# Optimization experiments

Measured on AMD Instinct MI355X. Metric: run time of the kernel, lower is better.

The kernel has to match this reference:

```python
import jax, jax.numpy as jnp
import numpy as np

LAMBDA_ENTROPY = 0.1
LAMBDA_REPULSION = 0.5
LAMBDA_INTER = 0.3
TEMPERATURE = 1.0
EPS = 1e-8


def setup_inputs() -> dict:
    key = jax.random.key(0)
    k1, k2 = jax.random.split(key)
    membership = jax.random.uniform(k1, (16384, 64, 32), dtype=jnp.float32)   # (N,F,K) soft bin assignments
    teacher_preds = jax.random.uniform(k2, (16384, 128), dtype=jnp.float32)   # (N,C)
    return {"membership": membership, "teacher_preds": teacher_preds}


def reference(membership, teacher_preds):
    N, F, K = membership.shape
    # --- weighted centroids per (feature, bin) ---
    bin_mass = membership.sum(axis=0) + EPS                       # (F,K)
    sum_weighted_y = jnp.einsum('nfk,nc->fkc', membership, teacher_preds)  # avoids (N,F,K,C)
    centroids = sum_weighted_y / bin_mass[..., None]              # (F,K,C)
    # --- weighted intra-bin variance: ||y_n - c_fk||^2 expanded, no (N,F,K,C) tensor ---
    y_sq = jnp.sum(teacher_preds * teacher_preds, axis=-1)        # (N,)
    c_sq = jnp.sum(centroids * centroids, axis=-1)                # (F,K)
    cross = jnp.einsum('nc,fkc->nfk', teacher_preds, centroids)   # (N,F,K)
    dist_sq = y_sq[:, None, None] + c_sq[None, :, :] - 2.0 * cross
    weighted_variance = jnp.sum(membership * dist_sq, axis=0) / bin_mass  # (F,K)
    loss_dispersion = weighted_variance.sum()
    # --- bin-occupancy entropy ---
    p_bins = bin_mass / N                                         # (F,K)
    loss_entropy = jnp.sum(p_bins * jnp.log(p_bins + EPS))
    # --- neighbor repulsion between adjacent bin centroids ---
    neighbor_dist = jnp.sum((centroids[:, :-1, :] - centroids[:, 1:, :]) ** 2, axis=-1)  # (F,K-1)
    loss_repulsion = jnp.sum(jnp.exp(-neighbor_dist / TEMPERATURE))
    # --- all-pairs inter-bin dispersion, batched over F (replaces python loop) ---
    dots = jnp.einsum('fkc,fjc->fkj', centroids, centroids)       # (F,K,K)
    pairwise = c_sq[:, :, None] + c_sq[:, None, :] - 2.0 * dots
    triu = jnp.triu(jnp.ones((K, K), dtype=centroids.dtype), k=1)  # strictly upper
    loss_inter = jnp.sum(jnp.exp(-pairwise / TEMPERATURE) * triu) / F
    total = (loss_dispersion
             + LAMBDA_ENTROPY * loss_entropy
             + LAMBDA_REPULSION * loss_repulsion
             + LAMBDA_INTER * loss_inter)
    return total, loss_dispersion, loss_entropy, loss_repulsion, loss_inter
```

## Files before the change

### kernel.cpp

```cpp
#include <hip/hip_runtime.h>
#include <math.h>

#define N_PTS   16384
#define F_DIM   64
#define K_BINS  32
#define C_DIM   128
#define FK      2048
#define NB32    (N_PTS / 32)
#define CW      132
#define EPS_F   1e-8f
#define NCHUNK  16
#define CN      1024

typedef _Float16 f16x8 __attribute__((ext_vector_type(8)));
typedef float    f32x4 __attribute__((ext_vector_type(4)));

__global__ __launch_bounds__(256) void build_ybf_k(const float* __restrict__ Y,
                                                   _Float16* __restrict__ Ybf,
                                                   float* __restrict__ accs) {
    __shared__ __align__(16) float Yl[64][132];
    __shared__ float ysql[64];
    const int t  = threadIdx.x;
    if (blockIdx.x == 0 && t < 8) accs[t] = 0.0f;
    const int n0 = blockIdx.x * 64;
    const int nl = t >> 5;
    const int c4 = t & 31;
#pragma unroll
    for (int p = 0; p < 8; ++p) {
        const int n = p * 8 + nl;
        const float4 v = reinterpret_cast<const float4*>(Y + (size_t)(n0 + n) * C_DIM)[c4];
        reinterpret_cast<float4*>(Yl[n])[c4] = v;
        float sq = v.x * v.x + v.y * v.y + v.z * v.z + v.w * v.w;
#pragma unroll
        for (int m = 16; m >= 1; m >>= 1) sq += __shfl_xor(sq, m, 64);
        if (c4 == 0) ysql[n] = sq;
    }
    __syncthreads();
    for (int p = 0; p < 5; ++p) {
        const int s = t + p * 256;
        if (s < 1152) {
            const int nb2  = s / 576;
            const int r    = s % 576;
            const int ct   = r >> 6;
            const int l    = r & 63;
            const int quad = l >> 4, cl = l & 15;
            const int nloc = nb2 * 32 + quad * 8;
            f16x8 v;
            if (ct < 8) {
                const int c = ct * 16 + cl;
#pragma unroll
                for (int j = 0; j < 8; ++j) v[j] = (_Float16)Yl[nloc + j][c];
            } else if (cl == 0) {
#pragma unroll
                for (int j = 0; j < 8; ++j) v[j] = (_Float16)ysql[nloc + j];
            } else if (cl == 1) {
#pragma unroll
                for (int j = 0; j < 8; ++j) v[j] = (_Float16)1.0f;
            } else {
#pragma unroll
                for (int j = 0; j < 8; ++j) v[j] = (_Float16)0.0f;
            }
            const int nb = blockIdx.x * 2 + nb2;
            *reinterpret_cast<f16x8*>(Ybf + ((size_t)(ct * NB32 + nb) * 64 + l) * 8) = v;
        }
    }
}

__global__ __launch_bounds__(256) void gemm_k(const float* __restrict__ M,
                                              const _Float16* __restrict__ Ybf,
                                              float* __restrict__ wpart) {
    __shared__ __align__(16) _Float16 Bb[2][2][9][512];
    const int t    = threadIdx.x;
    const int fk0  = blockIdx.x * 32;
    const int ch   = blockIdx.y;
    const int w    = t >> 6;
    const int g    = w >> 1;
    const int wl   = w & 1;
    const int l    = t & 63;
    const int quad = l >> 4;
    const int cl   = l & 15;
    const int fkA  = fk0 + wl * 16 + cl;
    const float* mp = M + fkA;
    const int n0   = ch * CN + g * 512;
    const int nb0  = n0 >> 5;

    f32x4 acc[9] = {};
    float a0r[8], a1r[8];

#define STAGE(s, par)                                                          \
    {                                                                          \
        const int nb_ = nb0 + (s);                                             \
        _Pragma("unroll")                                                      \
        for (int ct = wl; ct < 9; ct += 2) {                                   \
            const _Float16* g_ = Ybf + ((size_t)(ct * NB32 + nb_) * 64 + l) * 8; \
            __builtin_amdgcn_global_load_lds(                                  \
                (const __attribute__((address_space(1))) unsigned*)g_,         \
                (__attribute__((address_space(3))) unsigned*)&Bb[g][par][ct][0], \
                16, 0, 0);                                                     \
        }                                                                      \
    }
#define LOADA(ar, s)                                                           \
    {                                                                          \
        const size_t nbase_ = (size_t)(n0 + (s) * 32 + quad * 8);              \
        _Pragma("unroll")                                                      \
        for (int j = 0; j < 8; ++j) ar[j] = mp[(nbase_ + j) * FK];             \
    }

    STAGE(0, 0); LOADA(a0r, 0);
    STAGE(1, 1); LOADA(a1r, 1);

    for (int s = 0; s < 16; s += 2) {
        __syncthreads();
        {
            f16x8 bf[9];
#pragma unroll
            for (int ct = 0; ct < 9; ++ct)
                bf[ct] = *reinterpret_cast<const f16x8*>(&Bb[g][0][ct][l * 8]);
            f16x8 af;
#pragma unroll
            for (int j = 0; j < 8; ++j) af[j] = (_Float16)a0r[j];
            __syncthreads();
            if (s + 2 < 16) { STAGE(s + 2, 0); LOADA(a0r, s + 2); }
#pragma unroll
            for (int ct = 0; ct < 9; ++ct)
                acc[ct] = __builtin_amdgcn_mfma_f32_16x16x32_f16(af, bf[ct], acc[ct], 0, 0, 0);
        }
        __syncthreads();
        {
            f16x8 bf[9];
#pragma unroll
            for (int ct = 0; ct < 9; ++ct)
                bf[ct] = *reinterpret_cast<const f16x8*>(&Bb[g][1][ct][l * 8]);
            f16x8 af;
#pragma unroll
            for (int j = 0; j < 8; ++j) af[j] = (_Float16)a1r[j];
            __syncthreads();
            if (s + 3 < 16) { STAGE(s + 3, 1); LOADA(a1r, s + 3); }
#pragma unroll
            for (int ct = 0; ct < 9; ++ct)
                acc[ct] = __builtin_amdgcn_mfma_f32_16x16x32_f16(af, bf[ct], acc[ct], 0, 0, 0);
        }
    }
#undef STAGE
#undef LOADA

    float* scr = reinterpret_cast<float*>(&Bb[0][0][0][0]);
    if (g == 1) {
#pragma unroll
        for (int ct = 0; ct < 9; ++ct)
#pragma unroll
            for (int r = 0; r < 4; ++r)
                scr[(wl * 16 + quad * 4 + r) * 144 + ct * 16 + cl] = acc[ct][r];
    }
    __syncthreads();
    if (g == 0) {
        float* wp = wpart + (size_t)ch * FK * CW;
#pragma unroll
        for (int ct = 0; ct < 9; ++ct) {
            const int c = ct * 16 + cl;
            if (c < CW) {
#pragma unroll
                for (int r = 0; r < 4; ++r) {
                    const int row = wl * 16 + quad * 4 + r;
                    const int fk  = fk0 + row;
                    wp[(size_t)fk * CW + c] = acc[ct][r] + scr[row * 144 + c];
                }
            }
        }
    }
}

__global__ __launch_bounds__(128) void reduce_w_k(const float* __restrict__ wpart,
                                                  float* __restrict__ W, int nchunk) {
    const int idx = blockIdx.x * 128 + threadIdx.x;
    const float4* src = reinterpret_cast<const float4*>(wpart);
    const size_t cs = (size_t)FK * CW / 4;
    float4 s0 = make_float4(0.f, 0.f, 0.f, 0.f), s1 = s0, s2 = s0, s3 = s0;
    int ch = 0;
    for (; ch + 3 < nchunk; ch += 4) {
        const float4 a = src[idx + (size_t)(ch + 0) * cs];
        const float4 b = src[idx + (size_t)(ch + 1) * cs];
        const float4 c = src[idx + (size_t)(ch + 2) * cs];
        const float4 d = src[idx + (size_t)(ch + 3) * cs];
        s0.x += a.x; s0.y += a.y; s0.z += a.z; s0.w += a.w;
        s1.x += b.x; s1.y += b.y; s1.z += b.z; s1.w += b.w;
        s2.x += c.x; s2.y += c.y; s2.z += c.z; s2.w += c.w;
        s3.x += d.x; s3.y += d.y; s3.z += d.z; s3.w += d.w;
    }
    for (; ch < nchunk; ++ch) {
        const float4 a = src[idx + (size_t)ch * cs];
        s0.x += a.x; s0.y += a.y; s0.z += a.z; s0.w += a.w;
    }
    float4 r;
    r.x = (s0.x + s1.x) + (s2.x + s3.x);
    r.y = (s0.y + s1.y) + (s2.y + s3.y);
    r.z = (s0.z + s1.z) + (s2.z + s3.z);
    r.w = (s0.w + s1.w) + (s2.w + s3.w);
    reinterpret_cast<float4*>(W)[idx] = r;
}

__global__ __launch_bounds__(256) void epilogue_k(const float* __restrict__ W,
                                                  float* __restrict__ accs,
                                                  float* __restrict__ out) {
    __shared__ __align__(16) float Wl[32][CW];
    __shared__ float Bv[32], Binv[32], S1v[32], csq[32];
    __shared__ float scr[32][8];
    __shared__ float4 red4[256];
    const int t = threadIdx.x;
    const int f = blockIdx.x;

    for (int e = t; e < 32 * 33; e += 256) {
        const int k = e / 33, c4 = e % 33;
        reinterpret_cast<float4*>(Wl[k])[c4] =
            reinterpret_cast<const float4*>(W + (size_t)(f * 32 + k) * CW)[c4];
    }
    __syncthreads();
    if (t < 32) {
        const float B = Wl[t][129] + EPS_F;
        Bv[t] = B; Binv[t] = 1.0f / B; S1v[t] = Wl[t][128];
    }
    __syncthreads();
    {
        const int k = t >> 3, g = t & 7;
        const float ib = Binv[k];
        float s = 0.f;
        for (int c = g * 16; c < g * 16 + 16; ++c) {
            const float v = Wl[k][c] * ib;
            Wl[k][c] = v;
            s = fmaf(v, v, s);
        }
        scr[k][g] = s;
    }
    __syncthreads();
    if (t < 32) {
        float s = 0.f;
#pragma unroll
        for (int g = 0; g < 8; ++g) s += scr[t][g];
        csq[t] = s;
    }
    __syncthreads();

    float my_disp = 0.f, my_ent = 0.f, my_rep = 0.f, my_inter = 0.f;
    if (t < 32) {
        my_disp = (S1v[t] - csq[t] * (Bv[t] + EPS_F)) * Binv[t];
        const float p = Bv[t] * (1.0f / (float)N_PTS);
        my_ent = p * logf(p + EPS_F);
    }
    {
        const int pr = t >> 3, g = t & 7;
        float s = 0.f;
        if (pr < 31) {
            for (int c = g * 16; c < g * 16 + 16; ++c) {
                const float d = Wl[pr][c] - Wl[pr + 1][c];
                s = fmaf(d, d, s);
            }
        }
        __syncthreads();
        scr[pr][g] = s;
    }
    __syncthreads();
    if (t < 31) {
        float d = 0.f;
#pragma unroll
        for (int g = 0; g < 8; ++g) d += scr[t][g];
        my_rep = expf(-d);
    }
#pragma unroll
    for (int s4 = 0; s4 < 4; ++s4) {
        const int slot = t + s4 * 256;
        const int k = slot >> 5, j = slot & 31;
        if (k < j) {
            float dot = 0.f;
            for (int c4 = 0; c4 < 32; ++c4) {
                const float4 a = reinterpret_cast<const float4*>(Wl[k])[c4];
                const float4 b = reinterpret_cast<const float4*>(Wl[j])[c4];
                dot = fmaf(a.x, b.x, dot); dot = fmaf(a.y, b.y, dot);
                dot = fmaf(a.z, b.z, dot); dot = fmaf(a.w, b.w, dot);
            }
            my_inter += expf(-(csq[k] + csq[j] - 2.0f * dot));
        }
    }
    red4[t] = make_float4(my_disp, my_ent, my_rep, my_inter);
    __syncthreads();
    for (int off = 128; off >= 1; off >>= 1) {
        if (t < off) {
            const float4 a = red4[t], b = red4[t + off];
            red4[t] = make_float4(a.x + b.x, a.y + b.y, a.z + b.z, a.w + b.w);
        }
        __syncthreads();
    }
    if (t == 0) {
        atomicAdd(accs + 0, red4[0].x);
        atomicAdd(accs + 1, red4[0].y);
        atomicAdd(accs + 2, red4[0].z);
        atomicAdd(accs + 3, red4[0].w);
        __threadfence();
        const unsigned prev = __hip_atomic_fetch_add(
            reinterpret_cast<unsigned*>(accs + 4), 1u,
            __ATOMIC_ACQ_REL, __HIP_MEMORY_SCOPE_AGENT);
        if (prev == (unsigned)(F_DIM - 1)) {
            const float disp = __hip_atomic_load(accs + 0, __ATOMIC_RELAXED, __HIP_MEMORY_SCOPE_AGENT);
            const float ent  = __hip_atomic_load(accs + 1, __ATOMIC_RELAXED, __HIP_MEMORY_SCOPE_AGENT);
            const float rep  = __hip_atomic_load(accs + 2, __ATOMIC_RELAXED, __HIP_MEMORY_SCOPE_AGENT);
            const float inter = __hip_atomic_load(accs + 3, __ATOMIC_RELAXED, __HIP_MEMORY_SCOPE_AGENT)
                                * (1.0f / (float)F_DIM);
            out[0] = disp + 0.1f * ent + 0.5f * rep + 0.3f * inter;
            out[1] = disp;
            out[2] = ent;
            out[3] = rep;
            out[4] = inter;
        }
    }
}

extern "C" void kernel_launch(void* const* d_in, const int* in_sizes, int n_in,
                              void* d_out, int out_size, void* d_ws, size_t ws_size,
                              hipStream_t stream) {
    const float* M = (const float*)d_in[0];
    const float* Y = (const float*)d_in[1];
    float* out = (float*)d_out;
    char*  ws  = (char*)d_ws;

    const size_t ybfBytes = (size_t)9 * NB32 * 64 * 8 * sizeof(_Float16);
    const size_t wBytes   = (size_t)FK * CW * sizeof(float);

    _Float16* Ybf   = (_Float16*)ws;
    float*    W     = (float*)(ws + ybfBytes);
    float*    accs  = (float*)(ws + ybfBytes + wBytes);
    float*    wpart = (float*)(ws + ybfBytes + wBytes + 1024);

    build_ybf_k<<<dim3(N_PTS / 64), dim3(256), 0, stream>>>(Y, Ybf, accs);
    gemm_k<<<dim3(64, NCHUNK), dim3(256), 0, stream>>>(M, Ybf, wpart);
    reduce_w_k<<<dim3(FK * CW / 4 / 128), dim3(128), 0, stream>>>(wpart, W, NCHUNK);
    epilogue_k<<<dim3(F_DIM), dim3(256), 0, stream>>>(W, accs, out);
}
```

Baseline: 238.0 us.

## Deepen A-operand prefetch to three stages with explicit vmcnt waits and sched barriers

After: 234.5 us. About the same (-1.4%).

```diff
diff --git a/kernel.cpp b/kernel.cpp
--- a/kernel.cpp
+++ b/kernel.cpp
@@ -85,8 +85,9 @@
     const int nb0  = n0 >> 5;
 
     f32x4 acc[9] = {};
-    float a0r[8], a1r[8];
-
+    float ar[3][8];
+
+#define WAITVM(n) asm volatile("s_waitcnt vmcnt(" #n ")" ::: "memory")
 #define STAGE(s, par)                                                          \
     {                                                                          \
         const int nb_ = nb0 + (s);                                             \
@@ -99,51 +100,51 @@
                 16, 0, 0);                                                     \
         }                                                                      \
     }
-#define LOADA(ar, s)                                                           \
+#define LOADA(s)                                                               \
     {                                                                          \
         const size_t nbase_ = (size_t)(n0 + (s) * 32 + quad * 8);              \
         _Pragma("unroll")                                                      \
-        for (int j = 0; j < 8; ++j) ar[j] = mp[(nbase_ + j) * FK];             \
-    }
-
-    STAGE(0, 0); LOADA(a0r, 0);
-    STAGE(1, 1); LOADA(a1r, 1);
-
-    for (int s = 0; s < 16; s += 2) {
-        __syncthreads();
-        {
-            f16x8 bf[9];
-#pragma unroll
-            for (int ct = 0; ct < 9; ++ct)
-                bf[ct] = *reinterpret_cast<const f16x8*>(&Bb[g][0][ct][l * 8]);
-            f16x8 af;
-#pragma unroll
-            for (int j = 0; j < 8; ++j) af[j] = (_Float16)a0r[j];
-            __syncthreads();
-            if (s + 2 < 16) { STAGE(s + 2, 0); LOADA(a0r, s + 2); }
-#pragma unroll
-            for (int ct = 0; ct < 9; ++ct)
-                acc[ct] = __builtin_amdgcn_mfma_f32_16x16x32_f16(af, bf[ct], acc[ct], 0, 0, 0);
-        }
-        __syncthreads();
-        {
-            f16x8 bf[9];
-#pragma unroll
-            for (int ct = 0; ct < 9; ++ct)
-                bf[ct] = *reinterpret_cast<const f16x8*>(&Bb[g][1][ct][l * 8]);
-            f16x8 af;
-#pragma unroll
-            for (int j = 0; j < 8; ++j) af[j] = (_Float16)a1r[j];
-            __syncthreads();
-            if (s + 3 < 16) { STAGE(s + 3, 1); LOADA(a1r, s + 3); }
-#pragma unroll
-            for (int ct = 0; ct < 9; ++ct)
-                acc[ct] = __builtin_amdgcn_mfma_f32_16x16x32_f16(af, bf[ct], acc[ct], 0, 0, 0);
-        }
-    }
+        for (int j = 0; j < 8; ++j) ar[(s) % 3][j] = mp[(nbase_ + j) * FK];    \
+    }
+#define SBAR0() __builtin_amdgcn_sched_barrier(0)
+
+    STAGE(0, 0); SBAR0(); LOADA(0); SBAR0();
+    STAGE(1, 1); SBAR0(); LOADA(1); SBAR0(); LOADA(2); SBAR0();
+
+#pragma unroll
+    for (int s = 0; s < 16; ++s) {
+        if (s < 14)       WAITVM(20);
+        else if (s == 14) WAITVM(12);
+        else              WAITVM(0);
+        __builtin_amdgcn_s_barrier();
+        SBAR0();
+        f16x8 bf[9];
+#pragma unroll
+        for (int ct = 0; ct < 9; ++ct)
+            bf[ct] = *reinterpret_cast<const f16x8*>(&Bb[g][s & 1][ct][l * 8]);
+        f16x8 af;
+#pragma unroll
+        for (int j = 0; j < 8; ++j) af[j] = (_Float16)ar[s % 3][j];
+        asm volatile("s_waitcnt lgkmcnt(0)" ::: "memory");
+        SBAR0();
+        __builtin_amdgcn_s_barrier();
+        SBAR0();
+        if (s + 2 < 16) STAGE(s + 2, s & 1);
+        SBAR0();
+        if (s + 3 < 16) LOADA(s + 3);
+        SBAR0();
+        __builtin_amdgcn_s_setprio(1);
+#pragma unroll
+        for (int ct = 0; ct < 9; ++ct)
+            acc[ct] = __builtin_amdgcn_mfma_f32_16x16x32_f16(af, bf[ct], acc[ct], 0, 0, 0);
+        __builtin_amdgcn_s_setprio(0);
+    }
+#undef WAITVM
 #undef STAGE
 #undef LOADA
-
+#undef SBAR0
+
+    __syncthreads();
     float* scr = reinterpret_cast<float*>(&Bb[0][0][0][0]);
     if (g == 1) {
 #pragma unroll
```

## Stage membership tiles into LDS via async global_load_lds and size chunks from workspace

Applied to the files above, without the earlier changes.

Result: no change. 237.7 us (-0.1%).

```diff
diff --git a/kernel.cpp b/kernel.cpp
--- a/kernel.cpp
+++ b/kernel.cpp
@@ -9,8 +9,6 @@
 #define NB32    (N_PTS / 32)
 #define CW      132
 #define EPS_F   1e-8f
-#define NCHUNK  16
-#define CN      1024
 
 typedef _Float16 f16x8 __attribute__((ext_vector_type(8)));
 typedef float    f32x4 __attribute__((ext_vector_type(4)));
@@ -68,7 +66,9 @@
 
 __global__ __launch_bounds__(256) void gemm_k(const float* __restrict__ M,
                                               const _Float16* __restrict__ Ybf,
-                                              float* __restrict__ wpart) {
+                                              float* __restrict__ wpart,
+                                              int cn) {
+    __shared__ __align__(16) float    At[2][2][32][32];
     __shared__ __align__(16) _Float16 Bb[2][2][9][512];
     const int t    = threadIdx.x;
     const int fk0  = blockIdx.x * 32;
@@ -79,13 +79,11 @@
     const int l    = t & 63;
     const int quad = l >> 4;
     const int cl   = l & 15;
-    const int fkA  = fk0 + wl * 16 + cl;
-    const float* mp = M + fkA;
-    const int n0   = ch * CN + g * 512;
+    const int n0   = ch * cn + g * (cn >> 1);
     const int nb0  = n0 >> 5;
+    const int steps = cn >> 6;
 
     f32x4 acc[9] = {};
-    float a0r[8], a1r[8];
 
 #define STAGE(s, par)                                                          \
     {                                                                          \
@@ -98,18 +96,22 @@
                 (__attribute__((address_space(3))) unsigned*)&Bb[g][par][ct][0], \
                 16, 0, 0);                                                     \
         }                                                                      \
-    }
-#define LOADA(ar, s)                                                           \
-    {                                                                          \
-        const size_t nbase_ = (size_t)(n0 + (s) * 32 + quad * 8);              \
         _Pragma("unroll")                                                      \
-        for (int j = 0; j < 8; ++j) ar[j] = mp[(nbase_ + j) * FK];             \
-    }
-
-    STAGE(0, 0); LOADA(a0r, 0);
-    STAGE(1, 1); LOADA(a1r, 1);
-
-    for (int s = 0; s < 16; s += 2) {
+        for (int ii = 0; ii < 2; ++ii) {                                       \
+            const int i = wl * 2 + ii;                                         \
+            const float* gA = M + (size_t)(n0 + (s) * 32 + i * 8 + (l >> 3)) * FK \
+                              + fk0 + (l & 7) * 4;                             \
+            __builtin_amdgcn_global_load_lds(                                  \
+                (const __attribute__((address_space(1))) unsigned*)gA,         \
+                (__attribute__((address_space(3))) unsigned*)&At[g][par][i * 8][0], \
+                16, 0, 0);                                                     \
+        }                                                                      \
+    }
+
+    STAGE(0, 0);
+    STAGE(1, 1);
+
+    for (int s = 0; s < steps; s += 2) {
         __syncthreads();
         {
             f16x8 bf[9];
@@ -118,9 +120,10 @@
                 bf[ct] = *reinterpret_cast<const f16x8*>(&Bb[g][0][ct][l * 8]);
             f16x8 af;
 #pragma unroll
-            for (int j = 0; j < 8; ++j) af[j] = (_Float16)a0r[j];
+            for (int j = 0; j < 8; ++j)
+                af[j] = (_Float16)At[g][0][quad * 8 + j][wl * 16 + cl];
             __syncthreads();
-            if (s + 2 < 16) { STAGE(s + 2, 0); LOADA(a0r, s + 2); }
+            if (s + 2 < steps) STAGE(s + 2, 0);
 #pragma unroll
             for (int ct = 0; ct < 9; ++ct)
                 acc[ct] = __builtin_amdgcn_mfma_f32_16x16x32_f16(af, bf[ct], acc[ct], 0, 0, 0);
@@ -133,16 +136,16 @@
                 bf[ct] = *reinterpret_cast<const f16x8*>(&Bb[g][1][ct][l * 8]);
             f16x8 af;
 #pragma unroll
-            for (int j = 0; j < 8; ++j) af[j] = (_Float16)a1r[j];
+            for (int j = 0; j < 8; ++j)
+                af[j] = (_Float16)At[g][1][quad * 8 + j][wl * 16 + cl];
             __syncthreads();
-            if (s + 3 < 16) { STAGE(s + 3, 1); LOADA(a1r, s + 3); }
+            if (s + 3 < steps) STAGE(s + 3, 1);
 #pragma unroll
             for (int ct = 0; ct < 9; ++ct)
                 acc[ct] = __builtin_amdgcn_mfma_f32_16x16x32_f16(af, bf[ct], acc[ct], 0, 0, 0);
         }
     }
 #undef STAGE
-#undef LOADA
 
     float* scr = reinterpret_cast<float*>(&Bb[0][0][0][0]);
     if (g == 1) {
@@ -329,8 +332,13 @@
     float*    accs  = (float*)(ws + ybfBytes + wBytes);
     float*    wpart = (float*)(ws + ybfBytes + wBytes + 1024);
 
+    const size_t used = ybfBytes + wBytes + 1024;
+    int nchunk = 16;
+    while (nchunk > 1 && used + (size_t)nchunk * wBytes > ws_size) nchunk >>= 1;
+    const int cn = N_PTS / nchunk;
+
     build_ybf_k<<<dim3(N_PTS / 64), dim3(256), 0, stream>>>(Y, Ybf, accs);
-    gemm_k<<<dim3(64, NCHUNK), dim3(256), 0, stream>>>(M, Ybf, wpart);
-    reduce_w_k<<<dim3(FK * CW / 4 / 128), dim3(128), 0, stream>>>(wpart, W, NCHUNK);
+    gemm_k<<<dim3(64, nchunk), dim3(256), 0, stream>>>(M, Ybf, wpart, cn);
+    reduce_w_k<<<dim3(FK * CW / 4 / 128), dim3(128), 0, stream>>>(wpart, W, nchunk);
     epilogue_k<<<dim3(F_DIM), dim3(256), 0, stream>>>(W, accs, out);
 }
```
